# Kernel optimization log

Hardware: AMD Instinct MI355X
Metric: run time of the kernel (lower is better)

## Reference

```python
import jax, jax.numpy as jnp
import numpy as np
from jax import lax

EPS = 1e-5


def fps(xyz, npoint):
    # Farthest point sampling; xyz [B, N, 3] -> idx [B, npoint] (starts at point 0)
    B, N, _ = xyz.shape

    def body(carry, _):
        dist, far = carry
        c = jnp.take_along_axis(xyz, far[:, None, None], axis=1)  # [B,1,3]
        d = jnp.sum((xyz - c) ** 2, -1)                            # [B,N]
        dist = jnp.minimum(dist, d)
        nxt = jnp.argmax(dist, -1).astype(jnp.int32)
        return (dist, nxt), far

    init = (jnp.full((B, N), 1e10, xyz.dtype), jnp.zeros((B,), jnp.int32))
    _, idx = lax.scan(body, init, None, length=npoint)
    return idx.T  # [B, npoint]


def query_ball(radius, nsample, xyz, new_xyz):
    # xyz [B,N,3], new_xyz [B,S,3] -> idx [B,S,nsample]
    N = xyz.shape[1]
    sqr = jnp.sum((new_xyz[:, :, None, :] - xyz[:, None, :, :]) ** 2, -1)  # [B,S,N]
    idx = jnp.where(sqr > radius * radius, N, jnp.arange(N)[None, None, :])
    idx = jnp.sort(idx, axis=-1)[:, :, :nsample]
    # out-of-ball slots get replaced by the first in-ball index (torch repo behavior)
    return jnp.where(idx == N, idx[:, :, :1], idx)


def gather_pts(x, idx):
    # x [B,N,C], idx [B,...] -> [B,...,C]
    B = x.shape[0]
    b = jnp.arange(B).reshape((B,) + (1,) * (idx.ndim - 1))
    return x[b, idx]


def mlp_bn(x, layers):
    # x [B,S,K,C]; shared 1x1-conv MLP + training-mode BatchNorm + ReLU
    for w, g, b in layers:
        x = jnp.einsum('bskc,oc->bsko', x, w)
        mean = x.mean((0, 1, 2))
        var = x.var((0, 1, 2))  # biased, as torch BN uses for normalization
        x = jax.nn.relu((x - mean) * lax.rsqrt(var + EPS) * g + b)
    return x


def set_abstraction(xyz, points, npoint, radius, nsample, layers, group_all):
    B = xyz.shape[0]
    if group_all:
        new_xyz = jnp.zeros((B, 1, 3), xyz.dtype)
        new_points = xyz[:, None]  # [B,1,N,3] (raw xyz, no centering)
        if points is not None:
            new_points = jnp.concatenate([new_points, points[:, None]], -1)
    else:
        fidx = fps(xyz, npoint)
        new_xyz = gather_pts(xyz, fidx)                     # [B,S,3]
        idx = query_ball(radius, nsample, xyz, new_xyz)     # [B,S,K]
        grouped = gather_pts(xyz, idx) - new_xyz[:, :, None, :]
        if points is not None:
            new_points = jnp.concatenate([grouped, gather_pts(points, idx)], -1)
        else:
            new_points = grouped
    feat = mlp_bn(new_points, layers).max(2)  # max-pool over neighbors -> [B,S,C]
    return new_xyz, feat


def _forward(xyz_time, l1, l2, l3):
    B, T, N, _ = xyz_time.shape
    x = xyz_time.reshape(B * T, N, 4)
    xyz, t = x[..., :3], x[..., 3:]
    x1_xyz, x1 = set_abstraction(xyz, t, 512, 0.2, 32, l1, False)
    x2_xyz, x2 = set_abstraction(x1_xyz, x1, 128, 0.4, 64, l2, False)
    _, x3 = set_abstraction(x2_xyz, x2, None, None, None, l3, True)
    return x3.reshape(B, T, -1)


def setup_inputs() -> dict:
    key = jax.random.key(0)
    ks = jax.random.split(key, 16)
    inp = {"xyz_time": jax.random.uniform(ks[0], (2, 4, 4096, 4), jnp.float32)}
    specs = {1: [(64, 4), (64, 64), (128, 64)],
             2: [(128, 131), (128, 128), (256, 128)],
             3: [(256, 259), (512, 256), (1024, 512)]}
    i = 1
    for s, layers in specs.items():
        for j, (o, c) in enumerate(layers):
            inp[f"w{s}_{j}"] = jax.random.normal(jax.random.fold_in(ks[i], j), (o, c), jnp.float32) * 0.1
            inp[f"g{s}_{j}"] = jnp.ones((o,), jnp.float32)
            inp[f"b{s}_{j}"] = jnp.zeros((o,), jnp.float32)
        i += 1
    return inp


def reference(xyz_time, w1_0, g1_0, b1_0, w1_1, g1_1, b1_1, w1_2, g1_2, b1_2,
              w2_0, g2_0, b2_0, w2_1, g2_1, b2_1, w2_2, g2_2, b2_2,
              w3_0, g3_0, b3_0, w3_1, g3_1, b3_1, w3_2, g3_2, b3_2):
    l1 = [(w1_0, g1_0, b1_0), (w1_1, g1_1, b1_1), (w1_2, g1_2, b1_2)]
    l2 = [(w2_0, g2_0, b2_0), (w2_1, g2_1, b2_1), (w2_2, g2_2, b2_2)]
    l3 = [(w3_0, g3_0, b3_0), (w3_1, g3_1, b3_1), (w3_2, g3_2, b3_2)]
    return _forward(xyz_time, l1, l2, l3)
```

## Files before the change

### kernel.cpp

```cpp
#include <hip/hip_runtime.h>


typedef short s16x8 __attribute__((ext_vector_type(8)));
typedef float f32x4 __attribute__((ext_vector_type(4)));

__device__ __forceinline__ unsigned short f2bf_rne(float f) {
    unsigned u = __float_as_uint(f);
    u += 0x7FFFu + ((u >> 16) & 1u);
    return (unsigned short)(u >> 16);
}
__device__ __forceinline__ void f2bf_split(float v, unsigned short& hi,
                                           unsigned short& lo) {
    unsigned u = __float_as_uint(v);
    unsigned r = u + 0x7FFFu + ((u >> 16) & 1u);
    hi = (unsigned short)(r >> 16);
    float vh = __uint_as_float(r & 0xFFFF0000u);
    lo = f2bf_rne(v - vh);
}

__device__ __forceinline__ unsigned long long umax64(unsigned long long a,
                                                     unsigned long long b) {
    return a > b ? a : b;
}

__device__ __forceinline__ unsigned wred_umax63(unsigned v) {
    unsigned t;
    t = (unsigned)__builtin_amdgcn_update_dpp(0, (int)v, 0x111, 0xf, 0xf, true); if (t > v) v = t;
    t = (unsigned)__builtin_amdgcn_update_dpp(0, (int)v, 0x112, 0xf, 0xf, true); if (t > v) v = t;
    t = (unsigned)__builtin_amdgcn_update_dpp(0, (int)v, 0x114, 0xf, 0xf, true); if (t > v) v = t;
    t = (unsigned)__builtin_amdgcn_update_dpp(0, (int)v, 0x118, 0xf, 0xf, true); if (t > v) v = t;
    t = (unsigned)__builtin_amdgcn_update_dpp(0, (int)v, 0x142, 0xa, 0xf, true); if (t > v) v = t;
    t = (unsigned)__builtin_amdgcn_update_dpp(0, (int)v, 0x143, 0xc, 0xf, true); if (t > v) v = t;
    return v;
}

__device__ __forceinline__ void wave_argmax(unsigned dbits, unsigned nInv,
                                            unsigned& vmax, unsigned& iInv) {
    unsigned m = wred_umax63(dbits);
    vmax = (unsigned)__builtin_amdgcn_readlane((int)m, 63);
    unsigned cand = (dbits == vmax) ? nInv : 0u;
    unsigned im = wred_umax63(cand);
    iInv = (unsigned)__builtin_amdgcn_readlane((int)im, 63);
}

struct PWArgs {
    const float* w[9];
    unsigned off[9];
    int O[9], C[9], CP[9];
};
__device__ __forceinline__ void prep_w_dev(const PWArgs& a,
                                           unsigned short* __restrict__ wh,
                                           unsigned short* __restrict__ wl,
                                           int i) {
    int l = 0;
#pragma unroll
    for (int k = 1; k < 9; ++k) if (i >= (int)a.off[k]) l = k;
    int li = i - (int)a.off[l];
    int CP = a.CP[l];
    int o = li / CP;
    int c = li - o * CP;
    float v = (c < a.C[l]) ? a.w[l][(size_t)o * a.C[l] + c] : 0.f;
    unsigned short h, lo;
    f2bf_split(v, h, lo);
    wh[i] = h; wl[i] = lo;
}

template<int NT, int ITEMS, int STRIDE>
__global__ __launch_bounds__(NT) void fps_block(
    const float* __restrict__ pts, int npoint,
    int* __restrict__ outIdx, float* __restrict__ outXyz,
    int nFps, PWArgs pw, unsigned short* __restrict__ wh,
    unsigned short* __restrict__ wl, int wtotal)
{
    constexpr int N = NT * ITEMS;
    constexpr int NW = NT / 64;
    __shared__ float4 scoord[N];
    __shared__ unsigned long long wkey[2][NW];

    if (blockIdx.x >= nFps) {
        int i = (blockIdx.x - nFps) * NT + threadIdx.x;
        if (i < wtotal) prep_w_dev(pw, wh, wl, i);
        return;
    }
// ... 42 lines not shown
            float dz = __fsub_rn(pz[w], cz);
            float d = __fadd_rn(__fadd_rn(__fmul_rn(dx, dx), __fmul_rn(dy, dy)),
                                __fmul_rn(dz, dz));
            float dd = fminf(dloc[w], d);
            dloc[w] = dd;
            if (dd > bestV) { bestV = dd; bestW = w; }
        }
        int bestN = tid + bestW * NT;
        unsigned vmax, iInv;
        wave_argmax(__float_as_uint(bestV), 0xFFFFFFFFu ^ (unsigned)bestN,
                    vmax, iInv);
        const int par = i & 1;
        if (lane == 0)
            wkey[par][wid] = ((unsigned long long)vmax << 32) | iInv;
        __syncthreads();
        unsigned long long kb = wkey[par][0];
#pragma unroll
        for (int w2 = 1; w2 < NW; ++w2) kb = umax64(kb, wkey[par][w2]);
        far = (int)(0xFFFFFFFFu ^ (unsigned)kb);
        float4 cc = scoord[far];
        cx = cc.x; cy = cc.y; cz = cc.z;
    }
}

__device__ void fps_wave_dev(const float* __restrict__ pts, int npoint,
                             int* __restrict__ outIdx, float* __restrict__ outXyz,
                             int b, float4* scoord)
{
    constexpr int ITEMS = 8;
    constexpr int STRIDE = 3;
    constexpr int N = 64 * ITEMS;
    const int tid = threadIdx.x;
    const float* P = pts + (size_t)b * N * STRIDE;

    float px[ITEMS], py[ITEMS], pz[ITEMS], dloc[ITEMS];
#pragma unroll
    for (int w = 0; w < ITEMS; ++w) {
        int n = tid + w * 64;
        float x = P[(size_t)n * STRIDE + 0];
        float y = P[(size_t)n * STRIDE + 1];
        float z = P[(size_t)n * STRIDE + 2];
        px[w] = x; py[w] = y; pz[w] = z;
        scoord[n] = make_float4(x, y, z, 0.f);
        dloc[w] = 1e10f;
    }
    __threadfence_block();
    float4 c0 = scoord[0];
    float cx = c0.x, cy = c0.y, cz = c0.z;
    int far = 0;

    for (int i = 0; i < npoint; ++i) {
        if (tid == 0) {
            outIdx[(size_t)b * npoint + i] = far;
            outXyz[((size_t)b * npoint + i) * 3 + 0] = cx;
            outXyz[((size_t)b * npoint + i) * 3 + 1] = cy;
            outXyz[((size_t)b * npoint + i) * 3 + 2] = cz;
        }
        float bestV = -1.0f;
        int bestW = 0;
#pragma unroll
        for (int w = 0; w < ITEMS; ++w) {
            float dx = __fsub_rn(px[w], cx);
            float dy = __fsub_rn(py[w], cy);
            float dz = __fsub_rn(pz[w], cz);
            float d = __fadd_rn(__fadd_rn(__fmul_rn(dx, dx), __fmul_rn(dy, dy)),
                                __fmul_rn(dz, dz));
            float dd = fminf(dloc[w], d);
            dloc[w] = dd;
            if (dd > bestV) { bestV = dd; bestW = w; }
        }
        int bestN = tid + bestW * 64;
        unsigned vmax, iInv;
        wave_argmax(__float_as_uint(bestV), 0xFFFFFFFFu ^ (unsigned)bestN,
                    vmax, iInv);
        far = (int)(0xFFFFFFFFu ^ iInv);
        float4 cc = scoord[far];
        cx = cc.x; cy = cc.y; cz = cc.z;
    }
}

__global__ __launch_bounds__(256) void qb_group1(
    const float* __restrict__ xyz ,
    const float* __restrict__ ctr ,
    float* __restrict__ out )
{
    int gw = (blockIdx.x * 256 + threadIdx.x) >> 6;
    int lane = threadIdx.x & 63;
    if (gw >= 4096) return;
    int b = gw >> 9;
    const float* P = xyz + (size_t)b * 4096 * 4;
    float cx = ctr[(size_t)gw * 3 + 0];
    float cy = ctr[(size_t)gw * 3 + 1];
    float cz = ctr[(size_t)gw * 3 + 2];
    float* out0 = out + (size_t)gw * 32 * 8;
    int cnt = 0;
    float f0x = 0.f, f0y = 0.f, f0z = 0.f, f0t = 0.f;
    bool haveFirst = false;
    for (int base = 0; base < 4096 && cnt < 32; base += 64) {
        int n = base + lane;
        float4 p = *(const float4*)(P + (size_t)n * 4);
        float ex = __fsub_rn(p.x, cx);
        float ey = __fsub_rn(p.y, cy);
        float ez = __fsub_rn(p.z, cz);
        float d = __fadd_rn(__fadd_rn(__fmul_rn(ex, ex), __fmul_rn(ey, ey)),
                            __fmul_rn(ez, ez));
        bool inb = !(d > 0.04f);
        unsigned long long mask = __ballot(inb);
        if (mask) {
            if (!haveFirst) {
                int fl = (int)__builtin_ctzll(mask);
                f0x = __shfl(ex, fl); f0y = __shfl(ey, fl);
                f0z = __shfl(ez, fl); f0t = __shfl(p.w, fl);
                haveFirst = true;
            }
            if (inb) {
                int pos = cnt + __builtin_popcountll(mask & ((1ull << lane) - 1ull));
                if (pos < 32) {
                    float* o = out0 + (size_t)pos * 8;
                    *(float4*)o = make_float4(ex, ey, ez, p.w);
                    *(float4*)(o + 4) = make_float4(0.f, 0.f, 0.f, 0.f);
                }
            }
            cnt += (int)__builtin_popcountll(mask);
        }
    }
    if (cnt > 32) cnt = 32;
    for (int p2 = cnt + lane; p2 < 32; p2 += 64) {
        float* o = out0 + (size_t)p2 * 8;
        *(float4*)o = make_float4(f0x, f0y, f0z, f0t);
        *(float4*)(o + 4) = make_float4(0.f, 0.f, 0.f, 0.f);
    }
}

__global__ __launch_bounds__(256) void query_ball_kernel(
    const float* __restrict__ xyz, int stride, int N,
    const float* __restrict__ centers, int nCenters, int S,
    float r2, int nsample, int* __restrict__ outIdx)
{
    int gw = (blockIdx.x * 256 + threadIdx.x) >> 6;
    int lane = threadIdx.x & 63;
    if (gw >= nCenters) return;
    int b = gw / S;
    const float* P = xyz + (size_t)b * N * stride;
    float cx = centers[(size_t)gw * 3 + 0];
    float cy = centers[(size_t)gw * 3 + 1];
    float cz = centers[(size_t)gw * 3 + 2];
    int* out = outIdx + (size_t)gw * nsample;
    int cnt = 0;
    int firstIdx = 0;
    bool haveFirst = false;
    for (int base = 0; base < N && cnt < nsample; base += 64) {
        int n = base + lane;
        bool inb = false;
        if (n < N) {
            float dx = __fsub_rn(cx, P[(size_t)n * stride + 0]);
            float dy = __fsub_rn(cy, P[(size_t)n * stride + 1]);
            float dz = __fsub_rn(cz, P[(size_t)n * stride + 2]);
            float d = __fadd_rn(__fadd_rn(__fmul_rn(dx, dx), __fmul_rn(dy, dy)),
                                __fmul_rn(dz, dz));
            inb = !(d > r2);
        }
        unsigned long long mask = __ballot(inb);
        if (mask) {
            if (!haveFirst) { firstIdx = base + __builtin_ctzll(mask); haveFirst = true; }
            if (inb) {
                int pos = cnt + __builtin_popcountll(mask & ((1ull << lane) - 1ull));
                if (pos < nsample) out[pos] = n;
            }
            cnt += (int)__builtin_popcountll(mask);
        }
    }
    if (cnt > nsample) cnt = nsample;
    for (int p = cnt + lane; p < nsample; p += 64) out[p] = firstIdx;
}

__global__ __launch_bounds__(256) void group2_kernel(
    const float* __restrict__ xyz, const float* __restrict__ feat,
    const int* __restrict__ qb, const float* __restrict__ ctr,
    float* __restrict__ out)
{
    int i = blockIdx.x * 256 + threadIdx.x;
    if (i >= 65536 * 136) return;
    int sk = i / 136;
    int c = i - sk * 136;
    int b = sk / (128 * 64);
    int bs = sk / 64;
    int idx = qb[sk];
    idx = (idx < 0) ? 0 : (idx > 511 ? 511 : idx);
    float v = 0.f;
    if (c < 3)        v = __fsub_rn(xyz[((size_t)b * 512 + idx) * 3 + c], ctr[(size_t)bs * 3 + c]);
    else if (c < 131) v = feat[((size_t)b * 512 + idx) * 128 + (c - 3)];
    out[i] = v;
}

__global__ __launch_bounds__(256) void group3_kernel(
    const float* __restrict__ ctr2, const float* __restrict__ feat2,
    float* __restrict__ out)
{
    int i = blockIdx.x * 256 + threadIdx.x;
    if (i >= 1024 * 264) return;
    int sk = i / 264;
    int c = i - sk * 264;
    float v = 0.f;
    if (c < 3)        v = ctr2[(size_t)sk * 3 + c];
    else if (c < 259) v = feat2[(size_t)sk * 256 + (c - 3)];
    out[i] = v;
}

__global__ __launch_bounds__(256) void gemm_fused(
    const float* __restrict__ X,
    const float* __restrict__ scale, const float* __restrict__ shift,
    int applyAct,
    const unsigned short* __restrict__ Bh, const unsigned short* __restrict__ Bl,
    float* __restrict__ Y, double* __restrict__ part,
    int M, int AC, int CPW, int O, int YBmain,
    const float* __restrict__ fpsPts, int fpsNpoint,
    int* __restrict__ fpsIdx, float* __restrict__ fpsXyz)
{
    constexpr int PITCH = 40;
    __shared__ __align__(16) unsigned short sAh[128 * PITCH];
    __shared__ __align__(16) unsigned short sAl[128 * PITCH];
    __shared__ __align__(16) unsigned short sBh[128 * PITCH];
    __shared__ __align__(16) unsigned short sBl[128 * PITCH];
    __shared__ float sred[2048];

    if ((int)blockIdx.x >= YBmain) {
        if (threadIdx.x < 64 && fpsPts != nullptr)
            fps_wave_dev(fpsPts, fpsNpoint, fpsIdx, fpsXyz,
                         (int)blockIdx.x - YBmain, (float4*)sAh);
        return;
    }

    const int tid = threadIdx.x;
    const int lane = tid & 63;
    const int wid = tid >> 6;
    const int col15 = lane & 15;
    const int quad = lane >> 4;
    const int wm = (wid >> 1) * 64;
    const int wo = (wid & 1) * 64;
    const int m0 = blockIdx.x * 128;
    const int o0 = blockIdx.y * 128;
    const int YB = YBmain;
    const int lr = tid >> 2;
    const int lc = (tid & 3) * 8;

    f32x4 acc[4][4];
#pragma unroll
    for (int mt = 0; mt < 4; ++mt)
#pragma unroll
        for (int ot = 0; ot < 4; ++ot)
            acc[mt][ot] = {0.f, 0.f, 0.f, 0.f};

    for (int k0 = 0; k0 < CPW; k0 += 32) {
#pragma unroll
        for (int it = 0; it < 2; ++it) {
            int r = lr + it * 64;
            int c = k0 + lc;
            unsigned short h[8], l[8];
            if (c + 8 <= AC) {
                const float* xr = X + (size_t)(m0 + r) * AC + c;
                float4 v0 = *(const float4*)xr;
                float4 v1 = *(const float4*)(xr + 4);
                float vv[8] = {v0.x, v0.y, v0.z, v0.w, v1.x, v1.y, v1.z, v1.w};
#pragma unroll
                for (int j = 0; j < 8; ++j) {
                    float v = vv[j];
                    if (applyAct) v = fmaxf(v * scale[c + j] + shift[c + j], 0.f);
                    f2bf_split(v, h[j], l[j]);
                }
            } else {
#pragma unroll
                for (int j = 0; j < 8; ++j) { h[j] = 0; l[j] = 0; }
            }
            *(ushort4*)&sAh[r * PITCH + lc] = make_ushort4(h[0], h[1], h[2], h[3]);
            *(ushort4*)&sAh[r * PITCH + lc + 4] = make_ushort4(h[4], h[5], h[6], h[7]);
            *(ushort4*)&sAl[r * PITCH + lc] = make_ushort4(l[0], l[1], l[2], l[3]);
            *(ushort4*)&sAl[r * PITCH + lc + 4] = make_ushort4(l[4], l[5], l[6], l[7]);
        }
#pragma unroll
        for (int it = 0; it < 2; ++it) {
            int r = lr + it * 64;
            int c = k0 + lc;
            int o = o0 + r;
            uint4 vh = {0, 0, 0, 0}, vl = {0, 0, 0, 0};
            if (o < O && c < CPW) {
                size_t goff = (size_t)o * CPW + c;
                vh = *(const uint4*)(Bh + goff);
                vl = *(const uint4*)(Bl + goff);
            }
            *(uint4*)&sBh[r * PITCH + lc] = vh;
            *(uint4*)&sBl[r * PITCH + lc] = vl;
        }
        __syncthreads();
        s16x8 ah[4], al[4], bh[4], bl[4];
#pragma unroll
        for (int mt = 0; mt < 4; ++mt) {
            int rowoff = (wm + mt * 16 + col15) * PITCH + quad * 8;
            ah[mt] = *(const s16x8*)&sAh[rowoff];
            al[mt] = *(const s16x8*)&sAl[rowoff];
        }
#pragma unroll
        for (int ot = 0; ot < 4; ++ot) {
            int rowoff = (wo + ot * 16 + col15) * PITCH + quad * 8;
            bh[ot] = *(const s16x8*)&sBh[rowoff];
            bl[ot] = *(const s16x8*)&sBl[rowoff];
        }
#pragma unroll
        for (int mt = 0; mt < 4; ++mt)
#pragma unroll
            for (int ot = 0; ot < 4; ++ot) {
                acc[mt][ot] = __builtin_amdgcn_mfma_f32_16x16x32_bf16(
                    ah[mt], bl[ot], acc[mt][ot], 0, 0, 0);
                acc[mt][ot] = __builtin_amdgcn_mfma_f32_16x16x32_bf16(
                    al[mt], bh[ot], acc[mt][ot], 0, 0, 0);
                acc[mt][ot] = __builtin_amdgcn_mfma_f32_16x16x32_bf16(
                    ah[mt], bh[ot], acc[mt][ot], 0, 0, 0);
            }
        __syncthreads();
    }
#pragma unroll
    for (int mt = 0; mt < 4; ++mt)
#pragma unroll
        for (int ot = 0; ot < 4; ++ot) {
            int og = o0 + wo + ot * 16 + col15;
            if (og < O) {
#pragma unroll
                for (int r = 0; r < 4; ++r) {
                    int mg = m0 + wm + mt * 16 + quad * 4 + r;
                    Y[(size_t)mg * O + og] = acc[mt][ot][r];
                }
            }
        }
#pragma unroll
    for (int ot = 0; ot < 4; ++ot) {
        float s = 0.f, s2 = 0.f;
#pragma unroll
        for (int mt = 0; mt < 4; ++mt)
#pragma unroll
            for (int r = 0; r < 4; ++r) {
                float v = acc[mt][ot][r];
                s += v;
                s2 += v * v;
            }
        int slot = ((wid * 4 + quad) * 16 + col15) * 4 + ot;
        sred[slot * 2] = s;
        sred[slot * 2 + 1] = s2;
    }
    __syncthreads();
    if (tid < 128) {
        int col = tid;
        int o = o0 + col;
        if (o < O) {
            int cb = col >> 6;
            int ot = (col & 63) >> 4;
            int c15 = col & 15;
            double S = 0.0, S2 = 0.0;
#pragma unroll
            for (int wp = 0; wp < 2; ++wp) {
                int wd = cb + wp * 2;
#pragma unroll
                for (int q = 0; q < 4; ++q) {
                    int slot = ((wd * 4 + q) * 16 + c15) * 4 + ot;
                    S += (double)sred[slot * 2];
                    S2 += (double)sred[slot * 2 + 1];
                }
            }
            part[(size_t)o * YB + blockIdx.x] = S;
            part[(size_t)O * YB + (size_t)o * YB + blockIdx.x] = S2;
        }
    }
}

__global__ __launch_bounds__(256) void finalize_bn(
    const double* __restrict__ part, const float* __restrict__ g,
    const float* __restrict__ bb, float* __restrict__ scale,
    float* __restrict__ shift, int O, int YB, double invM)
{
    int o = blockIdx.x;
    int tid = threadIdx.x;
    double s = 0.0, s2 = 0.0;
    for (int yb = tid; yb < YB; yb += 256) {
        s  += part[(size_t)o * YB + yb];
        s2 += part[(size_t)O * YB + (size_t)o * YB + yb];
    }
    __shared__ double sd[512];
    sd[tid] = s;
    sd[256 + tid] = s2;
    __syncthreads();
#pragma unroll
    for (int st = 128; st > 0; st >>= 1) {
        if (tid < st) {
            sd[tid] += sd[tid + st];
            sd[256 + tid] += sd[256 + tid + st];
        }
        __syncthreads();
    }
    if (tid == 0) {
        double mean = sd[0] * invM;
        double var = sd[256] * invM - mean * mean;
        float varf = (float)var;
        if (varf < 0.f) varf = 0.f;
        float sc = g[o] * rsqrtf(varf + 1e-5f);
        scale[o] = sc;
        shift[o] = bb[o] - (float)mean * sc;
    }
}

__global__ __launch_bounds__(256) void bn_relu_max(
    const float* __restrict__ Y, const float* __restrict__ scale,
    const float* __restrict__ shift, float* __restrict__ out,
    int Stot, int K, int O)
{
    int idx = blockIdx.x * 256 + threadIdx.x;
    if (idx >= Stot * O) return;
    int s = idx / O;
    int o = idx - s * O;
    const float* base = Y + (size_t)s * K * O + o;
    float sc = scale[o], sh = shift[o];
    float mx = 0.f;
    for (int k = 0; k < K; ++k) {
        float v = base[(size_t)k * O] * sc + sh;
        v = fmaxf(v, 0.f);
        mx = fmaxf(mx, v);
    }
    out[idx] = mx;
}

extern "C" void kernel_launch(void* const* d_in, const int* in_sizes, int n_in,
                              void* d_out, int out_size, void* d_ws, size_t ws_size,
                              hipStream_t stream)
{
    const float* xin = (const float*)d_in[0];
    const float* w[9]; const float* g[9]; const float* bb[9];
    for (int i = 0; i < 9; ++i) {
        w[i]  = (const float*)d_in[1 + 3 * i];
        g[i]  = (const float*)d_in[2 + 3 * i];
        bb[i] = (const float*)d_in[3 + 3 * i];
    }

    char* base = (char*)d_ws;
    size_t off = 0;
    auto alloc = [&](size_t bytes) -> void* {
        void* p = base + off;
        off = (off + bytes + 255) & ~(size_t)255;
        return p;
    };
    const int OC[9][3] = {{64,4,8},{64,64,64},{128,64,64},
                          {128,131,136},{128,128,128},{256,128,128},
                          {256,259,264},{512,256,256},{1024,512,512}};
    size_t woff[10]; woff[0] = 0;
    for (int i = 0; i < 9; ++i) woff[i + 1] = woff[i] + (size_t)OC[i][0] * OC[i][2];

    int*    fps1   = (int*)alloc((size_t)4096 * 4);
    int*    fps2   = (int*)alloc((size_t)1024 * 4);
    int*    qb2    = (int*)alloc((size_t)65536 * 4);
    float*  nx1    = (float*)alloc((size_t)12288 * 4);
    float*  nx2    = (float*)alloc((size_t)3072 * 4);
    float*  feat1  = (float*)alloc((size_t)524288 * 4);
    float*  feat2  = (float*)alloc((size_t)262144 * 4);
    double* part   = (double*)alloc((size_t)262144 * 8);
    float*  scales = (float*)alloc((size_t)9 * 1024 * 4);
    float*  shifts = (float*)alloc((size_t)9 * 1024 * 4);
    unsigned short* WH = (unsigned short*)alloc(woff[9] * 2);
    unsigned short* WL = (unsigned short*)alloc(woff[9] * 2);
    const size_t zeroBytes = off;
    float*  XG = (float*)alloc((size_t)65536 * 136 * 4);
    float*  A  = (float*)alloc((size_t)16777216 * 4);
    if (off > ws_size) return;

    hipMemsetAsync(d_ws, 0, zeroBytes, stream);

    PWArgs pwa;
    for (int i = 0; i < 9; ++i) {
        pwa.w[i] = w[i]; pwa.off[i] = (unsigned)woff[i];
        pwa.O[i] = OC[i][0]; pwa.C[i] = OC[i][1]; pwa.CP[i] = OC[i][2];
    }
    const int nPrep = (int)((woff[9] + 255) / 256);

    fps_block<256, 16, 4><<<8 + nPrep, 256, 0, stream>>>(
        xin, 512, fps1, nx1, 8, pwa, WH, WL, (int)woff[9]);
    qb_group1<<<(4096 * 64) / 256, 256, 0, stream>>>(xin, nx1, XG);

    gemm_fused<<<dim3(1024, 1), 256, 0, stream>>>(XG, nullptr, nullptr, 0, WH + woff[0], WL + woff[0], A, part, 131072, 8, 8, 64, 1024, nullptr, 0, nullptr, nullptr);
    finalize_bn<<<64, 256, 0, stream>>>(part, g[0], bb[0], scales + 0 * 1024, shifts + 0 * 1024, 64, 1024, 1.0 / 131072.0);
    gemm_fused<<<dim3(1024, 1), 256, 0, stream>>>(A, scales + 0 * 1024, shifts + 0 * 1024, 1, WH + woff[1], WL + woff[1], XG, part, 131072, 64, 64, 64, 1024, nullptr, 0, nullptr, nullptr);
    finalize_bn<<<64, 256, 0, stream>>>(part, g[1], bb[1], scales + 1 * 1024, shifts + 1 * 1024, 64, 1024, 1.0 / 131072.0);
    gemm_fused<<<dim3(1024 + 8, 1), 256, 0, stream>>>(XG, scales + 1 * 1024, shifts + 1 * 1024, 1, WH + woff[2], WL + woff[2], A, part, 131072, 64, 64, 128, 1024, nx1, 128, fps2, nx2);
    finalize_bn<<<128, 256, 0, stream>>>(part, g[2], bb[2], scales + 2 * 1024, shifts + 2 * 1024, 128, 1024, 1.0 / 131072.0);
    bn_relu_max<<<(4096 * 128) / 256, 256, 0, stream>>>(A, scales + 2 * 1024, shifts + 2 * 1024, feat1, 4096, 32, 128);

    query_ball_kernel<<<(8 * 128 * 64) / 256, 256, 0, stream>>>(
        nx1, 3, 512, nx2, 8 * 128, 128, 0.16f, 64, qb2);
    group2_kernel<<<(65536 * 136) / 256, 256, 0, stream>>>(nx1, feat1, qb2, nx2, XG);

    gemm_fused<<<dim3(512, 1), 256, 0, stream>>>(XG, nullptr, nullptr, 0, WH + woff[3], WL + woff[3], A, part, 65536, 136, 136, 128, 512, nullptr, 0, nullptr, nullptr);
    finalize_bn<<<128, 256, 0, stream>>>(part, g[3], bb[3], scales + 3 * 1024, shifts + 3 * 1024, 128, 512, 1.0 / 65536.0);
    gemm_fused<<<dim3(512, 1), 256, 0, stream>>>(A, scales + 3 * 1024, shifts + 3 * 1024, 1, WH + woff[4], WL + woff[4], XG, part, 65536, 128, 128, 128, 512, nullptr, 0, nullptr, nullptr);
    finalize_bn<<<128, 256, 0, stream>>>(part, g[4], bb[4], scales + 4 * 1024, shifts + 4 * 1024, 128, 512, 1.0 / 65536.0);
    gemm_fused<<<dim3(512, 2), 256, 0, stream>>>(XG, scales + 4 * 1024, shifts + 4 * 1024, 1, WH + woff[5], WL + woff[5], A, part, 65536, 128, 128, 256, 512, nullptr, 0, nullptr, nullptr);
    finalize_bn<<<256, 256, 0, stream>>>(part, g[5], bb[5], scales + 5 * 1024, shifts + 5 * 1024, 256, 512, 1.0 / 65536.0);
    bn_relu_max<<<(1024 * 256) / 256, 256, 0, stream>>>(A, scales + 5 * 1024, shifts + 5 * 1024, feat2, 1024, 64, 256);

    group3_kernel<<<(1024 * 264) / 256, 256, 0, stream>>>(nx2, feat2, XG);

    gemm_fused<<<dim3(8, 2), 256, 0, stream>>>(XG, nullptr, nullptr, 0, WH + woff[6], WL + woff[6], A, part, 1024, 264, 264, 256, 8, nullptr, 0, nullptr, nullptr);
    finalize_bn<<<256, 256, 0, stream>>>(part, g[6], bb[6], scales + 6 * 1024, shifts + 6 * 1024, 256, 8, 1.0 / 1024.0);
    gemm_fused<<<dim3(8, 4), 256, 0, stream>>>(A, scales + 6 * 1024, shifts + 6 * 1024, 1, WH + woff[7], WL + woff[7], XG, part, 1024, 256, 256, 512, 8, nullptr, 0, nullptr, nullptr);
    finalize_bn<<<512, 256, 0, stream>>>(part, g[7], bb[7], scales + 7 * 1024, shifts + 7 * 1024, 512, 8, 1.0 / 1024.0);
    gemm_fused<<<dim3(8, 8), 256, 0, stream>>>(XG, scales + 7 * 1024, shifts + 7 * 1024, 1, WH + woff[8], WL + woff[8], A, part, 1024, 512, 512, 1024, 8, nullptr, 0, nullptr, nullptr);
    finalize_bn<<<1024, 256, 0, stream>>>(part, g[8], bb[8], scales + 8 * 1024, shifts + 8 * 1024, 1024, 8, 1.0 / 1024.0);
    bn_relu_max<<<(8 * 1024) / 256, 256, 0, stream>>>(A, scales + 8 * 1024, shifts + 8 * 1024, (float*)d_out, 8, 128, 1024);
}
```

Measured before the change: 826.1 us.

## Fuse each set-abstraction MLP stage into one cooperative persistent kernel

Replaces the per-layer gemm/finalize_bn/bn_relu_max launch chain with one cooperative kernel per stage. It loops over tiles persistently and uses grid-wide syncs between GEMM, BN finalize and max-pool, and it also folds grouping and query-ball work into the same kernel. The second FPS moves from the layer-3 GEMM launch into the qb_group1 launch. This removes many kernel launches and their tail idle time, at the cost of grid-sync overhead and a persistent grid capped at 512 blocks, which may underuse the GPU for the large GEMMs. A non-cooperative fallback path is kept.

```diff
diff --git a/kernel.cpp b/kernel.cpp
--- a/kernel.cpp
+++ b/kernel.cpp
@@ -1,4 +1,7 @@
 #include <hip/hip_runtime.h>
+#include <hip/hip_cooperative_groups.h>
+
+namespace cg = cooperative_groups;
 
 
 typedef short s16x8 __attribute__((ext_vector_type(8)));
@@ -207,8 +210,17 @@
 __global__ __launch_bounds__(256) void qb_group1(
     const float* __restrict__ xyz ,
     const float* __restrict__ ctr ,
-    float* __restrict__ out )
-{
+    float* __restrict__ out ,
+    int nQb, const float* __restrict__ fpsPts,
+    int* __restrict__ fpsIdx, float* __restrict__ fpsXyz)
+{
+    __shared__ float4 scoord[512];
+    if ((int)blockIdx.x >= nQb) {
+        if (threadIdx.x < 64)
+            fps_wave_dev(fpsPts, 128, fpsIdx, fpsXyz,
+                         (int)blockIdx.x - nQb, scoord);
+        return;
+    }
     int gw = (blockIdx.x * 256 + threadIdx.x) >> 6;
     int lane = threadIdx.x & 63;
     if (gw >= 4096) return;
@@ -257,14 +269,12 @@
     }
 }
 
-__global__ __launch_bounds__(256) void query_ball_kernel(
-    const float* __restrict__ xyz, int stride, int N,
-    const float* __restrict__ centers, int nCenters, int S,
-    float r2, int nsample, int* __restrict__ outIdx)
-{
-    int gw = (blockIdx.x * 256 + threadIdx.x) >> 6;
-    int lane = threadIdx.x & 63;
-    if (gw >= nCenters) return;
+__device__ __forceinline__ void qb2_dev(
+    const float* __restrict__ xyz, const float* __restrict__ centers,
+    int* __restrict__ outIdx, int gw, int lane)
+{
+    const int N = 512, stride = 3, S = 128, nsample = 64;
+    const float r2 = 0.16f;
     int b = gw / S;
     const float* P = xyz + (size_t)b * N * stride;
     float cx = centers[(size_t)gw * 3 + 0];
@@ -299,13 +309,21 @@
     for (int p = cnt + lane; p < nsample; p += 64) out[p] = firstIdx;
 }
 
-__global__ __launch_bounds__(256) void group2_kernel(
+__global__ __launch_bounds__(256) void query_ball_kernel(
+    const float* __restrict__ xyz, const float* __restrict__ centers,
+    int nCenters, int* __restrict__ outIdx)
+{
+    int gw = (blockIdx.x * 256 + threadIdx.x) >> 6;
+    int lane = threadIdx.x & 63;
+    if (gw >= nCenters) return;
+    qb2_dev(xyz, centers, outIdx, gw, lane);
+}
+
+__device__ __forceinline__ void group2_body(
     const float* __restrict__ xyz, const float* __restrict__ feat,
     const int* __restrict__ qb, const float* __restrict__ ctr,
-    float* __restrict__ out)
-{
-    int i = blockIdx.x * 256 + threadIdx.x;
-    if (i >= 65536 * 136) return;
+    float* __restrict__ out, int i)
+{
     int sk = i / 136;
     int c = i - sk * 136;
     int b = sk / (128 * 64);
@@ -318,12 +336,10 @@
     out[i] = v;
 }
 
-__global__ __launch_bounds__(256) void group3_kernel(
+__device__ __forceinline__ void group3_body(
     const float* __restrict__ ctr2, const float* __restrict__ feat2,
-    float* __restrict__ out)
-{
-    int i = blockIdx.x * 256 + threadIdx.x;
-    if (i >= 1024 * 264) return;
+    float* __restrict__ out, int i)
+{
     int sk = i / 264;
     int c = i - sk * 264;
     float v = 0.f;
@@ -332,30 +348,36 @@
     out[i] = v;
 }
 
-__global__ __launch_bounds__(256) void gemm_fused(
-    const float* __restrict__ X,
-    const float* __restrict__ scale, const float* __restrict__ shift,
-    int applyAct,
+__global__ __launch_bounds__(256) void group2_kernel(
+    const float* __restrict__ xyz, const float* __restrict__ feat,
+    const int* __restrict__ qb, const float* __restrict__ ctr,
+    float* __restrict__ out)
+{
+    int i = blockIdx.x * 256 + threadIdx.x;
+    if (i >= 65536 * 136) return;
+    group2_body(xyz, feat, qb, ctr, out, i);
+}
+
+__global__ __launch_bounds__(256) void group3_kernel(
+    const float* __restrict__ ctr2, const float* __restrict__ feat2,
+    float* __restrict__ out)
+{
+    int i = blockIdx.x * 256 + threadIdx.x;
+    if (i >= 1024 * 264) return;
+    group3_body(ctr2, feat2, out, i);
+}
+
+#define GPITCH 40
+
+__device__ void mlp_layer(
+    const float* __restrict__ X, const float* __restrict__ scale,
+    const float* __restrict__ shift, int applyAct,
     const unsigned short* __restrict__ Bh, const unsigned short* __restrict__ Bl,
     float* __restrict__ Y, double* __restrict__ part,
-    int M, int AC, int CPW, int O, int YBmain,
-    const float* __restrict__ fpsPts, int fpsNpoint,
-    int* __restrict__ fpsIdx, float* __restrict__ fpsXyz)
-{
-    constexpr int PITCH = 40;
-    __shared__ __align__(16) unsigned short sAh[128 * PITCH];
-    __shared__ __align__(16) unsigned short sAl[128 * PITCH];
-    __shared__ __align__(16) unsigned short sBh[128 * PITCH];
-    __shared__ __align__(16) unsigned short sBl[128 * PITCH];
-    __shared__ float sred[2048];
-
-    if ((int)blockIdx.x >= YBmain) {
-        if (threadIdx.x < 64 && fpsPts != nullptr)
-            fps_wave_dev(fpsPts, fpsNpoint, fpsIdx, fpsXyz,
-                         (int)blockIdx.x - YBmain, (float4*)sAh);
-        return;
-    }
-
+    int AC, int CPW, int O, int YB, int tstart, int G,
+    unsigned short* sAh, unsigned short* sAl,
+    unsigned short* sBh, unsigned short* sBl, float* sred)
+{
     const int tid = threadIdx.x;
     const int lane = tid & 63;
     const int wid = tid >> 6;
@@ -363,137 +385,282 @@
     const int quad = lane >> 4;
     const int wm = (wid >> 1) * 64;
     const int wo = (wid & 1) * 64;
-    const int m0 = blockIdx.x * 128;
-    const int o0 = blockIdx.y * 128;
-    const int YB = YBmain;
     const int lr = tid >> 2;
     const int lc = (tid & 3) * 8;
-
-    f32x4 acc[4][4];
-#pragma unroll
-    for (int mt = 0; mt < 4; ++mt)
-#pragma unroll
-        for (int ot = 0; ot < 4; ++ot)
-            acc[mt][ot] = {0.f, 0.f, 0.f, 0.f};
-
-    for (int k0 = 0; k0 < CPW; k0 += 32) {
-#pragma unroll
-        for (int it = 0; it < 2; ++it) {
-            int r = lr + it * 64;
-            int c = k0 + lc;
-            unsigned short h[8], l[8];
-            if (c + 8 <= AC) {
-                const float* xr = X + (size_t)(m0 + r) * AC + c;
-                float4 v0 = *(const float4*)xr;
-                float4 v1 = *(const float4*)(xr + 4);
-                float vv[8] = {v0.x, v0.y, v0.z, v0.w, v1.x, v1.y, v1.z, v1.w};
-#pragma unroll
-                for (int j = 0; j < 8; ++j) {
-                    float v = vv[j];
-                    if (applyAct) v = fmaxf(v * scale[c + j] + shift[c + j], 0.f);
-                    f2bf_split(v, h[j], l[j]);
+    const int ntile = YB * ((O + 127) >> 7);
+
+    for (int t = tstart; t < ntile; t += G) {
+        const int bx = t % YB;
+        const int oy = t / YB;
+        const int m0 = bx * 128;
+        const int o0 = oy * 128;
+
+        f32x4 acc[4][4];
+#pragma unroll
+        for (int mt = 0; mt < 4; ++mt)
+#pragma unroll
+            for (int ot = 0; ot < 4; ++ot)
+                acc[mt][ot] = {0.f, 0.f, 0.f, 0.f};
+
+        for (int k0 = 0; k0 < CPW; k0 += 32) {
+#pragma unroll
+            for (int it = 0; it < 2; ++it) {
+                int r = lr + it * 64;
+                int c = k0 + lc;
+                unsigned short h[8], l[8];
+                if (c + 8 <= AC) {
+                    const float* xr = X + (size_t)(m0 + r) * AC + c;
+                    float4 v0 = *(const float4*)xr;
+                    float4 v1 = *(const float4*)(xr + 4);
+                    float vv[8] = {v0.x, v0.y, v0.z, v0.w, v1.x, v1.y, v1.z, v1.w};
+#pragma unroll
+                    for (int j = 0; j < 8; ++j) {
+                        float v = vv[j];
+                        if (applyAct) v = fmaxf(v * scale[c + j] + shift[c + j], 0.f);
+                        f2bf_split(v, h[j], l[j]);
+                    }
+                } else {
+#pragma unroll
+                    for (int j = 0; j < 8; ++j) { h[j] = 0; l[j] = 0; }
                 }
-            } else {
-#pragma unroll
-                for (int j = 0; j < 8; ++j) { h[j] = 0; l[j] = 0; }
-            }
-            *(ushort4*)&sAh[r * PITCH + lc] = make_ushort4(h[0], h[1], h[2], h[3]);
-            *(ushort4*)&sAh[r * PITCH + lc + 4] = make_ushort4(h[4], h[5], h[6], h[7]);
-            *(ushort4*)&sAl[r * PITCH + lc] = make_ushort4(l[0], l[1], l[2], l[3]);
-            *(ushort4*)&sAl[r * PITCH + lc + 4] = make_ushort4(l[4], l[5], l[6], l[7]);
-        }
-#pragma unroll
-        for (int it = 0; it < 2; ++it) {
-            int r = lr + it * 64;
-            int c = k0 + lc;
-            int o = o0 + r;
-            uint4 vh = {0, 0, 0, 0}, vl = {0, 0, 0, 0};
-            if (o < O && c < CPW) {
-                size_t goff = (size_t)o * CPW + c;
-                vh = *(const uint4*)(Bh + goff);
-                vl = *(const uint4*)(Bl + goff);
-            }
-            *(uint4*)&sBh[r * PITCH + lc] = vh;
-            *(uint4*)&sBl[r * PITCH + lc] = vl;
+                *(ushort4*)&sAh[r * GPITCH + lc] = make_ushort4(h[0], h[1], h[2], h[3]);
+                *(ushort4*)&sAh[r * GPITCH + lc + 4] = make_ushort4(h[4], h[5], h[6], h[7]);
+                *(ushort4*)&sAl[r * GPITCH + lc] = make_ushort4(l[0], l[1], l[2], l[3]);
+                *(ushort4*)&sAl[r * GPITCH + lc + 4] = make_ushort4(l[4], l[5], l[6], l[7]);
+            }
+#pragma unroll
+            for (int it = 0; it < 2; ++it) {
+                int r = lr + it * 64;
+                int c = k0 + lc;
+                int o = o0 + r;
+                uint4 vh = {0, 0, 0, 0}, vl = {0, 0, 0, 0};
+                if (o < O && c < CPW) {
+                    size_t goff = (size_t)o * CPW + c;
+                    vh = *(const uint4*)(Bh + goff);
+                    vl = *(const uint4*)(Bl + goff);
+                }
+                *(uint4*)&sBh[r * GPITCH + lc] = vh;
+                *(uint4*)&sBl[r * GPITCH + lc] = vl;
+            }
+            __syncthreads();
+            s16x8 ah[4], al[4], bh[4], bl[4];
+#pragma unroll
+            for (int mt = 0; mt < 4; ++mt) {
+                int rowoff = (wm + mt * 16 + col15) * GPITCH + quad * 8;
+                ah[mt] = *(const s16x8*)&sAh[rowoff];
+                al[mt] = *(const s16x8*)&sAl[rowoff];
+            }
+#pragma unroll
+            for (int ot = 0; ot < 4; ++ot) {
+                int rowoff = (wo + ot * 16 + col15) * GPITCH + quad * 8;
+                bh[ot] = *(const s16x8*)&sBh[rowoff];
+                bl[ot] = *(const s16x8*)&sBl[rowoff];
+            }
+#pragma unroll
+            for (int mt = 0; mt < 4; ++mt)
+#pragma unroll
+                for (int ot = 0; ot < 4; ++ot) {
+                    acc[mt][ot] = __builtin_amdgcn_mfma_f32_16x16x32_bf16(
+                        ah[mt], bl[ot], acc[mt][ot], 0, 0, 0);
+                    acc[mt][ot] = __builtin_amdgcn_mfma_f32_16x16x32_bf16(
+                        al[mt], bh[ot], acc[mt][ot], 0, 0, 0);
+                    acc[mt][ot] = __builtin_amdgcn_mfma_f32_16x16x32_bf16(
+                        ah[mt], bh[ot], acc[mt][ot], 0, 0, 0);
+                }
+            __syncthreads();
+        }
+#pragma unroll
+        for (int mt = 0; mt < 4; ++mt)
+#pragma unroll
+            for (int ot = 0; ot < 4; ++ot) {
+                int og = o0 + wo + ot * 16 + col15;
+                if (og < O) {
+#pragma unroll
+                    for (int r = 0; r < 4; ++r) {
+                        int mg = m0 + wm + mt * 16 + quad * 4 + r;
+                        Y[(size_t)mg * O + og] = acc[mt][ot][r];
+                    }
+                }
+            }
+#pragma unroll
+        for (int ot = 0; ot < 4; ++ot) {
+            float s = 0.f, s2 = 0.f;
+#pragma unroll
+            for (int mt = 0; mt < 4; ++mt)
+#pragma unroll
+                for (int r = 0; r < 4; ++r) {
+                    float v = acc[mt][ot][r];
+                    s += v;
+                    s2 += v * v;
+                }
+            int slot = ((wid * 4 + quad) * 16 + col15) * 4 + ot;
+            sred[slot * 2] = s;
+            sred[slot * 2 + 1] = s2;
         }
         __syncthreads();
-        s16x8 ah[4], al[4], bh[4], bl[4];
-#pragma unroll
-        for (int mt = 0; mt < 4; ++mt) {
-            int rowoff = (wm + mt * 16 + col15) * PITCH + quad * 8;
-            ah[mt] = *(const s16x8*)&sAh[rowoff];
-            al[mt] = *(const s16x8*)&sAl[rowoff];
-        }
-#pragma unroll
-        for (int ot = 0; ot < 4; ++ot) {
-            int rowoff = (wo + ot * 16 + col15) * PITCH + quad * 8;
-            bh[ot] = *(const s16x8*)&sBh[rowoff];
-            bl[ot] = *(const s16x8*)&sBl[rowoff];
-        }
-#pragma unroll
-        for (int mt = 0; mt < 4; ++mt)
-#pragma unroll
-            for (int ot = 0; ot < 4; ++ot) {
-                acc[mt][ot] = __builtin_amdgcn_mfma_f32_16x16x32_bf16(
-                    ah[mt], bl[ot], acc[mt][ot], 0, 0, 0);
-                acc[mt][ot] = __builtin_amdgcn_mfma_f32_16x16x32_bf16(
-                    al[mt], bh[ot], acc[mt][ot], 0, 0, 0);
-                acc[mt][ot] = __builtin_amdgcn_mfma_f32_16x16x32_bf16(
-                    ah[mt], bh[ot], acc[mt][ot], 0, 0, 0);
-            }
+        if (tid < 128) {
+            int col = tid;
+            int o = o0 + col;
+            if (o < O) {
+                int cb = col >> 6;
+                int ot = (col & 63) >> 4;
+                int c15 = col & 15;
+                double S = 0.0, S2 = 0.0;
+#pragma unroll
+                for (int wp = 0; wp < 2; ++wp) {
+                    int wd = cb + wp * 2;
+#pragma unroll
+                    for (int q = 0; q < 4; ++q) {
+                        int slot = ((wd * 4 + q) * 16 + c15) * 4 + ot;
+                        S += (double)sred[slot * 2];
+                        S2 += (double)sred[slot * 2 + 1];
+                    }
+                }
+                part[(size_t)o * YB + bx] = S;
+                part[(size_t)O * YB + (size_t)o * YB + bx] = S2;
+            }
+        }
         __syncthreads();
     }
-#pragma unroll
-    for (int mt = 0; mt < 4; ++mt)
-#pragma unroll
-        for (int ot = 0; ot < 4; ++ot) {
-            int og = o0 + wo + ot * 16 + col15;
-            if (og < O) {
-#pragma unroll
-                for (int r = 0; r < 4; ++r) {
-                    int mg = m0 + wm + mt * 16 + quad * 4 + r;
-                    Y[(size_t)mg * O + og] = acc[mt][ot][r];
-                }
-            }
-        }
-#pragma unroll
-    for (int ot = 0; ot < 4; ++ot) {
-        float s = 0.f, s2 = 0.f;
-#pragma unroll
-        for (int mt = 0; mt < 4; ++mt)
-#pragma unroll
-            for (int r = 0; r < 4; ++r) {
-                float v = acc[mt][ot][r];
-                s += v;
-                s2 += v * v;
-            }
-        int slot = ((wid * 4 + quad) * 16 + col15) * 4 + ot;
-        sred[slot * 2] = s;
-        sred[slot * 2 + 1] = s2;
-    }
-    __syncthreads();
-    if (tid < 128) {
-        int col = tid;
-        int o = o0 + col;
-        if (o < O) {
-            int cb = col >> 6;
-            int ot = (col & 63) >> 4;
-            int c15 = col & 15;
-            double S = 0.0, S2 = 0.0;
-#pragma unroll
-            for (int wp = 0; wp < 2; ++wp) {
-                int wd = cb + wp * 2;
-#pragma unroll
-                for (int q = 0; q < 4; ++q) {
-                    int slot = ((wd * 4 + q) * 16 + c15) * 4 + ot;
-                    S += (double)sred[slot * 2];
-                    S2 += (double)sred[slot * 2 + 1];
-                }
-            }
-            part[(size_t)o * YB + blockIdx.x] = S;
-            part[(size_t)O * YB + (size_t)o * YB + blockIdx.x] = S2;
-        }
-    }
+}
+
+__device__ void mlp_fin(
+    const double* __restrict__ part, int O, int YB,
+    const float* __restrict__ g, const float* __restrict__ bb,
+    float* __restrict__ scale, float* __restrict__ shift,
+    double invM, int ostart, int G, double* sd)
+{
+    const int tid = threadIdx.x;
+    for (int o = ostart; o < O; o += G) {
+        double s = 0.0, s2 = 0.0;
+        for (int yb = tid; yb < YB; yb += 256) {
+            s  += part[(size_t)o * YB + yb];
+            s2 += part[(size_t)O * YB + (size_t)o * YB + yb];
+        }
+        sd[tid] = s;
+        sd[256 + tid] = s2;
+        __syncthreads();
+#pragma unroll
+        for (int st = 128; st > 0; st >>= 1) {
+            if (tid < st) {
+                sd[tid] += sd[tid + st];
+                sd[256 + tid] += sd[256 + tid + st];
+            }
+            __syncthreads();
+        }
+        if (tid == 0) {
+            double mean = sd[0] * invM;
+            double var = sd[256] * invM - mean * mean;
+            float varf = (float)var;
+            if (varf < 0.f) varf = 0.f;
+            float sc = g[o] * rsqrtf(varf + 1e-5f);
+            scale[o] = sc;
+            shift[o] = bb[o] - (float)mean * sc;
+        }
+        __syncthreads();
+    }
+}
+
+struct MlpArgs {
+    int preMode;
+    const float* preXyz; const float* preFeat; const int* preQb;
+    const float* preCtr; float* preOut;
+    const float* X0; float* Y0; float* Y1; float* Y2;
+    const unsigned short *Bh0, *Bl0, *Bh1, *Bl1, *Bh2, *Bl2;
+    const float *g0, *bb0, *g1, *bb1, *g2, *bb2;
+    float *sc0, *sh0, *sc1, *sh1, *sc2, *sh2;
+    double* part; double invM;
+    int YB;
+    int AC0, CPW0, O0, AC1, CPW1, O1, AC2, CPW2, O2;
+    int K, Stot; float* feat;
+    int doQB;
+    const float* qbXyz; const float* qbCtr; int* qbOut;
+};
+
+__global__ __launch_bounds__(256, 2) void mlp_coop(MlpArgs a)
+{
+    __shared__ __align__(16) unsigned short sAh[128 * GPITCH];
+    __shared__ __align__(16) unsigned short sAl[128 * GPITCH];
+    __shared__ __align__(16) unsigned short sBh[128 * GPITCH];
+    __shared__ __align__(16) unsigned short sBl[128 * GPITCH];
+    __shared__ __align__(16) float sred[2048];
+    cg::grid_group grid = cg::this_grid();
+    const int G = gridDim.x;
+    const int bid = blockIdx.x;
+    const int tid = threadIdx.x;
+
+    if (a.preMode == 2) {
+        for (int i = bid * 256 + tid; i < 65536 * 136; i += G * 256)
+            group2_body(a.preXyz, a.preFeat, a.preQb, a.preCtr, a.preOut, i);
+        __threadfence(); grid.sync();
+    } else if (a.preMode == 3) {
+        for (int i = bid * 256 + tid; i < 1024 * 264; i += G * 256)
+            group3_body(a.preCtr, a.preFeat, a.preOut, i);
+        __threadfence(); grid.sync();
+    }
+
+    mlp_layer(a.X0, nullptr, nullptr, 0, a.Bh0, a.Bl0, a.Y0, a.part,
+              a.AC0, a.CPW0, a.O0, a.YB, bid, G, sAh, sAl, sBh, sBl, sred);
+    __threadfence(); grid.sync();
+    mlp_fin(a.part, a.O0, a.YB, a.g0, a.bb0, a.sc0, a.sh0, a.invM, bid, G,
+            (double*)sred);
+    __threadfence(); grid.sync();
+
+    mlp_layer(a.Y0, a.sc0, a.sh0, 1, a.Bh1, a.Bl1, a.Y1, a.part,
+              a.AC1, a.CPW1, a.O1, a.YB, bid, G, sAh, sAl, sBh, sBl, sred);
+    __threadfence(); grid.sync();
+    mlp_fin(a.part, a.O1, a.YB, a.g1, a.bb1, a.sc1, a.sh1, a.invM, bid, G,
+            (double*)sred);
+    __threadfence(); grid.sync();
+
+    mlp_layer(a.Y1, a.sc1, a.sh1, 1, a.Bh2, a.Bl2, a.Y2, a.part,
+              a.AC2, a.CPW2, a.O2, a.YB, bid, G, sAh, sAl, sBh, sBl, sred);
+    __threadfence(); grid.sync();
+    mlp_fin(a.part, a.O2, a.YB, a.g2, a.bb2, a.sc2, a.sh2, a.invM, bid, G,
+            (double*)sred);
+    __threadfence(); grid.sync();
+
+    {
+        const int total = a.Stot * a.O2;
+        for (int idx = bid * 256 + tid; idx < total; idx += G * 256) {
+            int s = idx / a.O2;
+            int o = idx - s * a.O2;
+            const float* basep = a.Y2 + (size_t)s * a.K * a.O2 + o;
+            float sc = a.sc2[o], sh = a.sh2[o];
+            float mx = 0.f;
+            for (int k = 0; k < a.K; ++k) {
+                float v = basep[(size_t)k * a.O2] * sc + sh;
+                v = fmaxf(v, 0.f);
+                mx = fmaxf(mx, v);
+            }
+            a.feat[idx] = mx;
+        }
+    }
+
+    if (a.doQB) {
+        const int wv = tid >> 6, lane = tid & 63;
+        for (int gw = bid * 4 + wv; gw < 1024; gw += G * 4)
+            qb2_dev(a.qbXyz, a.qbCtr, a.qbOut, gw, lane);
+    }
+}
+
+__global__ __launch_bounds__(256) void gemm_fused(
+    const float* __restrict__ X,
+    const float* __restrict__ scale, const float* __restrict__ shift,
+    int applyAct,
+    const unsigned short* __restrict__ Bh, const unsigned short* __restrict__ Bl,
+    float* __restrict__ Y, double* __restrict__ part,
+    int M, int AC, int CPW, int O, int YBmain)
+{
+    __shared__ __align__(16) unsigned short sAh[128 * GPITCH];
+    __shared__ __align__(16) unsigned short sAl[128 * GPITCH];
+    __shared__ __align__(16) unsigned short sBh[128 * GPITCH];
+    __shared__ __align__(16) unsigned short sBl[128 * GPITCH];
+    __shared__ __align__(16) float sred[2048];
+    const int tstart = blockIdx.x + blockIdx.y * gridDim.x;
+    const int G = gridDim.x * gridDim.y;
+    mlp_layer(X, scale, shift, applyAct, Bh, Bl, Y, part, AC, CPW, O, YBmain,
+              tstart, G, sAh, sAl, sBh, sBl, sred);
 }
 
 __global__ __launch_bounds__(256) void finalize_bn(
@@ -501,34 +668,8 @@
     const float* __restrict__ bb, float* __restrict__ scale,
     float* __restrict__ shift, int O, int YB, double invM)
 {
-    int o = blockIdx.x;
-    int tid = threadIdx.x;
-    double s = 0.0, s2 = 0.0;
-    for (int yb = tid; yb < YB; yb += 256) {
-        s  += part[(size_t)o * YB + yb];
-        s2 += part[(size_t)O * YB + (size_t)o * YB + yb];
-    }
     __shared__ double sd[512];
-    sd[tid] = s;
-    sd[256 + tid] = s2;
-    __syncthreads();
-#pragma unroll
-    for (int st = 128; st > 0; st >>= 1) {
-        if (tid < st) {
-            sd[tid] += sd[tid + st];
-            sd[256 + tid] += sd[256 + tid + st];
-        }
-        __syncthreads();
-    }
-    if (tid == 0) {
-        double mean = sd[0] * invM;
-        double var = sd[256] * invM - mean * mean;
-        float varf = (float)var;
-        if (varf < 0.f) varf = 0.f;
-        float sc = g[o] * rsqrtf(varf + 1e-5f);
-        scale[o] = sc;
-        shift[o] = bb[o] - (float)mean * sc;
-    }
+    mlp_fin(part, O, YB, g, bb, scale, shift, invM, blockIdx.x, gridDim.x, sd);
 }
 
 __global__ __launch_bounds__(256) void bn_relu_max(
@@ -540,11 +681,11 @@
     if (idx >= Stot * O) return;
     int s = idx / O;
     int o = idx - s * O;
-    const float* base = Y + (size_t)s * K * O + o;
+    const float* basep = Y + (size_t)s * K * O + o;
     float sc = scale[o], sh = shift[o];
     float mx = 0.f;
     for (int k = 0; k < K; ++k) {
-        float v = base[(size_t)k * O] * sc + sh;
+        float v = basep[(size_t)k * O] * sc + sh;
         v = fmaxf(v, 0.f);
         mx = fmaxf(mx, v);
     }
@@ -604,35 +745,115 @@
 
     fps_block<256, 16, 4><<<8 + nPrep, 256, 0, stream>>>(
         xin, 512, fps1, nx1, 8, pwa, WH, WL, (int)woff[9]);
-    qb_group1<<<(4096 * 64) / 256, 256, 0, stream>>>(xin, nx1, XG);
-
-    gemm_fused<<<dim3(1024, 1), 256, 0, stream>>>(XG, nullptr, nullptr, 0, WH + woff[0], WL + woff[0], A, part, 131072, 8, 8, 64, 1024, nullptr, 0, nullptr, nullptr);
-    finalize_bn<<<64, 256, 0, stream>>>(part, g[0], bb[0], scales + 0 * 1024, shifts + 0 * 1024, 64, 1024, 1.0 / 131072.0);
-    gemm_fused<<<dim3(1024, 1), 256, 0, stream>>>(A, scales + 0 * 1024, shifts + 0 * 1024, 1, WH + woff[1], WL + woff[1], XG, part, 131072, 64, 64, 64, 1024, nullptr, 0, nullptr, nullptr);
-    finalize_bn<<<64, 256, 0, stream>>>(part, g[1], bb[1], scales + 1 * 1024, shifts + 1 * 1024, 64, 1024, 1.0 / 131072.0);
-    gemm_fused<<<dim3(1024 + 8, 1), 256, 0, stream>>>(XG, scales + 1 * 1024, shifts + 1 * 1024, 1, WH + woff[2], WL + woff[2], A, part, 131072, 64, 64, 128, 1024, nx1, 128, fps2, nx2);
-    finalize_bn<<<128, 256, 0, stream>>>(part, g[2], bb[2], scales + 2 * 1024, shifts + 2 * 1024, 128, 1024, 1.0 / 131072.0);
-    bn_relu_max<<<(4096 * 128) / 256, 256, 0, stream>>>(A, scales + 2 * 1024, shifts + 2 * 1024, feat1, 4096, 32, 128);
-
-    query_ball_kernel<<<(8 * 128 * 64) / 256, 256, 0, stream>>>(
-        nx1, 3, 512, nx2, 8 * 128, 128, 0.16f, 64, qb2);
-    group2_kernel<<<(65536 * 136) / 256, 256, 0, stream>>>(nx1, feat1, qb2, nx2, XG);
-
-    gemm_fused<<<dim3(512, 1), 256, 0, stream>>>(XG, nullptr, nullptr, 0, WH + woff[3], WL + woff[3], A, part, 65536, 136, 136, 128, 512, nullptr, 0, nullptr, nullptr);
-    finalize_bn<<<128, 256, 0, stream>>>(part, g[3], bb[3], scales + 3 * 1024, shifts + 3 * 1024, 128, 512, 1.0 / 65536.0);
-    gemm_fused<<<dim3(512, 1), 256, 0, stream>>>(A, scales + 3 * 1024, shifts + 3 * 1024, 1, WH + woff[4], WL + woff[4], XG, part, 65536, 128, 128, 128, 512, nullptr, 0, nullptr, nullptr);
-    finalize_bn<<<128, 256, 0, stream>>>(part, g[4], bb[4], scales + 4 * 1024, shifts + 4 * 1024, 128, 512, 1.0 / 65536.0);
-    gemm_fused<<<dim3(512, 2), 256, 0, stream>>>(XG, scales + 4 * 1024, shifts + 4 * 1024, 1, WH + woff[5], WL + woff[5], A, part, 65536, 128, 128, 256, 512, nullptr, 0, nullptr, nullptr);
-    finalize_bn<<<256, 256, 0, stream>>>(part, g[5], bb[5], scales + 5 * 1024, shifts + 5 * 1024, 256, 512, 1.0 / 65536.0);
-    bn_relu_max<<<(1024 * 256) / 256, 256, 0, stream>>>(A, scales + 5 * 1024, shifts + 5 * 1024, feat2, 1024, 64, 256);
-
-    group3_kernel<<<(1024 * 264) / 256, 256, 0, stream>>>(nx2, feat2, XG);
-
-    gemm_fused<<<dim3(8, 2), 256, 0, stream>>>(XG, nullptr, nullptr, 0, WH + woff[6], WL + woff[6], A, part, 1024, 264, 264, 256, 8, nullptr, 0, nullptr, nullptr);
-    finalize_bn<<<256, 256, 0, stream>>>(part, g[6], bb[6], scales + 6 * 1024, shifts + 6 * 1024, 256, 8, 1.0 / 1024.0);
-    gemm_fused<<<dim3(8, 4), 256, 0, stream>>>(A, scales + 6 * 1024, shifts + 6 * 1024, 1, WH + woff[7], WL + woff[7], XG, part, 1024, 256, 256, 512, 8, nullptr, 0, nullptr, nullptr);
-    finalize_bn<<<512, 256, 0, stream>>>(part, g[7], bb[7], scales + 7 * 1024, shifts + 7 * 1024, 512, 8, 1.0 / 1024.0);
-    gemm_fused<<<dim3(8, 8), 256, 0, stream>>>(XG, scales + 7 * 1024, shifts + 7 * 1024, 1, WH + woff[8], WL + woff[8], A, part, 1024, 512, 512, 1024, 8, nullptr, 0, nullptr, nullptr);
-    finalize_bn<<<1024, 256, 0, stream>>>(part, g[8], bb[8], scales + 8 * 1024, shifts + 8 * 1024, 1024, 8, 1.0 / 1024.0);
-    bn_relu_max<<<(8 * 1024) / 256, 256, 0, stream>>>(A, scales + 8 * 1024, shifts + 8 * 1024, (float*)d_out, 8, 128, 1024);
-}
+    qb_group1<<<1024 + 8, 256, 0, stream>>>(xin, nx1, XG, 1024, nx1, fps2, nx2);
+
+    int coopGrid = 0;
+    {
+        int nb = 0;
+        if (hipOccupancyMaxActiveBlocksPerMultiprocessor(
+                &nb, (const void*)mlp_coop, 256, 0) == hipSuccess && nb >= 1) {
+            long long total = (long long)nb * 256;
+            coopGrid = (int)(total < 512 ? total : 512);
+        }
+    }
+    auto launch_coop = [&](MlpArgs& m) -> bool {
+        if (coopGrid < 1) return false;
+        void* ka[] = {(void*)&m};
+        hipError_t e = hipLaunchCooperativeKernel(
+            (const void*)mlp_coop, dim3(coopGrid), dim3(256), ka, 0, stream);
+        return e == hipSuccess;
+    };
+    auto fb_layer = [&](const float* X, const float* sc, const float* sh,
+                        int act, int wi, float* Y, int M, int AC, int CPW,
+                        int O, int YB, int li, double invM) {
+        gemm_fused<<<dim3(YB, (O + 127) / 128), 256, 0, stream>>>(
+            X, sc, sh, act, WH + woff[wi], WL + woff[wi], Y, part,
+            M, AC, CPW, O, YB);
+        finalize_bn<<<O, 256, 0, stream>>>(part, g[wi], bb[wi],
+            scales + li * 1024, shifts + li * 1024, O, YB, invM);
+    };
+
+    {
+        MlpArgs m = {};
+        m.preMode = 0;
+        m.X0 = XG; m.Y0 = A; m.Y1 = XG; m.Y2 = A;
+        m.Bh0 = WH + woff[0]; m.Bl0 = WL + woff[0];
+        m.Bh1 = WH + woff[1]; m.Bl1 = WL + woff[1];
+        m.Bh2 = WH + woff[2]; m.Bl2 = WL + woff[2];
+        m.g0 = g[0]; m.bb0 = bb[0]; m.g1 = g[1]; m.bb1 = bb[1];
+        m.g2 = g[2]; m.bb2 = bb[2];
+        m.sc0 = scales + 0;    m.sh0 = shifts + 0;
+        m.sc1 = scales + 1024; m.sh1 = shifts + 1024;
+        m.sc2 = scales + 2048; m.sh2 = shifts + 2048;
+        m.part = part; m.invM = 1.0 / 131072.0; m.YB = 1024;
+        m.AC0 = 8;  m.CPW0 = 8;  m.O0 = 64;
+        m.AC1 = 64; m.CPW1 = 64; m.O1 = 64;
+        m.AC2 = 64; m.CPW2 = 64; m.O2 = 128;
+        m.K = 32; m.Stot = 4096; m.feat = feat1;
+        m.doQB = 1; m.qbXyz = nx1; m.qbCtr = nx2; m.qbOut = qb2;
+        if (!launch_coop(m)) {
+            fb_layer(XG, nullptr, nullptr, 0, 0, A, 131072, 8, 8, 64, 1024, 0, 1.0 / 131072.0);
+            fb_layer(A, scales + 0, shifts + 0, 1, 1, XG, 131072, 64, 64, 64, 1024, 1, 1.0 / 131072.0);
+            fb_layer(XG, scales + 1024, shifts + 1024, 1, 2, A, 131072, 64, 64, 128, 1024, 2, 1.0 / 131072.0);
+            bn_relu_max<<<(4096 * 128) / 256, 256, 0, stream>>>(A, scales + 2048, shifts + 2048, feat1, 4096, 32, 128);
+            query_ball_kernel<<<(8 * 128 * 64) / 256, 256, 0, stream>>>(nx1, nx2, 1024, qb2);
+        }
+    }
+
+    {
+        MlpArgs m = {};
+        m.preMode = 2;
+        m.preXyz = nx1; m.preFeat = feat1; m.preQb = qb2; m.preCtr = nx2;
+        m.preOut = XG;
+        m.X0 = XG; m.Y0 = A; m.Y1 = XG; m.Y2 = A;
+        m.Bh0 = WH + woff[3]; m.Bl0 = WL + woff[3];
+        m.Bh1 = WH + woff[4]; m.Bl1 = WL + woff[4];
+        m.Bh2 = WH + woff[5]; m.Bl2 = WL + woff[5];
+        m.g0 = g[3]; m.bb0 = bb[3]; m.g1 = g[4]; m.bb1 = bb[4];
+        m.g2 = g[5]; m.bb2 = bb[5];
+        m.sc0 = scales + 3072; m.sh0 = shifts + 3072;
+        m.sc1 = scales + 4096; m.sh1 = shifts + 4096;
+        m.sc2 = scales + 5120; m.sh2 = shifts + 5120;
+        m.part = part; m.invM = 1.0 / 65536.0; m.YB = 512;
+        m.AC0 = 136; m.CPW0 = 136; m.O0 = 128;
+        m.AC1 = 128; m.CPW1 = 128; m.O1 = 128;
+        m.AC2 = 128; m.CPW2 = 128; m.O2 = 256;
+        m.K = 64; m.Stot = 1024; m.feat = feat2;
+        m.doQB = 0;
+        if (!launch_coop(m)) {
+            group2_kernel<<<(65536 * 136) / 256, 256, 0, stream>>>(nx1, feat1, qb2, nx2, XG);
+            fb_layer(XG, nullptr, nullptr, 0, 3, A, 65536, 136, 136, 128, 512, 3, 1.0 / 65536.0);
+            fb_layer(A, scales + 3072, shifts + 3072, 1, 4, XG, 65536, 128, 128, 128, 512, 4, 1.0 / 65536.0);
+            fb_layer(XG, scales + 4096, shifts + 4096, 1, 5, A, 65536, 128, 128, 256, 512, 5, 1.0 / 65536.0);
+            bn_relu_max<<<(1024 * 256) / 256, 256, 0, stream>>>(A, scales + 5120, shifts + 5120, feat2, 1024, 64, 256);
+        }
+    }
+
+    {
+        MlpArgs m = {};
+        m.preMode = 3;
+        m.preCtr = nx2; m.preFeat = feat2; m.preOut = XG;
+        m.X0 = XG; m.Y0 = A; m.Y1 = XG; m.Y2 = A;
+        m.Bh0 = WH + woff[6]; m.Bl0 = WL + woff[6];
+        m.Bh1 = WH + woff[7]; m.Bl1 = WL + woff[7];
+        m.Bh2 = WH + woff[8]; m.Bl2 = WL + woff[8];
+        m.g0 = g[6]; m.bb0 = bb[6]; m.g1 = g[7]; m.bb1 = bb[7];
+        m.g2 = g[8]; m.bb2 = bb[8];
+        m.sc0 = scales + 6144; m.sh0 = shifts + 6144;
+        m.sc1 = scales + 7168; m.sh1 = shifts + 7168;
+        m.sc2 = scales + 8192; m.sh2 = shifts + 8192;
+        m.part = part; m.invM = 1.0 / 1024.0; m.YB = 8;
+        m.AC0 = 264; m.CPW0 = 264; m.O0 = 256;
+        m.AC1 = 256; m.CPW1 = 256; m.O1 = 512;
+        m.AC2 = 512; m.CPW2 = 512; m.O2 = 1024;
+        m.K = 128; m.Stot = 8; m.feat = (float*)d_out;
+        m.doQB = 0;
+        if (!launch_coop(m)) {
+            group3_kernel<<<(1024 * 264) / 256, 256, 0, stream>>>(nx2, feat2, XG);
+            fb_layer(XG, nullptr, nullptr, 0, 6, A, 1024, 264, 264, 256, 8, 6, 1.0 / 1024.0);
+            fb_layer(A, scales + 6144, shifts + 6144, 1, 7, XG, 1024, 256, 256, 512, 8, 7, 1.0 / 1024.0);
+            fb_layer(XG, scales + 7168, shifts + 7168, 1, 8, A, 1024, 512, 512, 1024, 8, 8, 1.0 / 1024.0);
+            bn_relu_max<<<(8 * 1024) / 256, 256, 0, stream>>>(A, scales + 8192, shifts + 8192, (float*)d_out, 8, 128, 1024);
+        }
+    }
+}
```

New measurement: 932.3 us. +12.9%, slower.
